# Kernel optimization log

Hardware: AMD Instinct MI355X
Metric: run time of the kernel (lower is better)

## Reference

```python
import jax, jax.numpy as jnp
import numpy as np
import math

NUM_HEADS = 16
WINDOW = 128  # telephone/sliding-window size: attend to self + previous WINDOW-1 tokens
EPS = 1e-6


def setup_inputs() -> dict:
    key = jax.random.key(0)
    k1, k2, k3, k4 = jax.random.split(key, 4)
    B, S, D = 4, 4096, 1024
    x = jax.random.normal(k1, (B, S, D), dtype=jnp.float32)
    g = jnp.ones((D,), dtype=jnp.float32)  # RMSNorm weight
    Wqkv = jax.random.normal(k2, (D, 3 * D), dtype=jnp.float32) * 0.02
    Wo = jax.random.normal(k3, (D, D), dtype=jnp.float32) * 0.02
    return {"x": x, "g": g, "Wqkv": Wqkv, "Wo": Wo}


def _telephone_block(x, g, Wqkv, Wo):
    B, S, D = x.shape
    H, dh, W = NUM_HEADS, D // NUM_HEADS, WINDOW
    nb = S // W  # number of key/query blocks

    # pre-RMSNorm
    xn = x * jax.lax.rsqrt(jnp.mean(x * x, axis=-1, keepdims=True) + EPS) * g

    # fused QKV projection
    qkv = xn @ Wqkv  # [B,S,3D]
    q, k, v = jnp.split(qkv, 3, axis=-1)

    def split_heads(t):
        # [B,S,D] -> [B,H,nb,W,dh]
        return t.reshape(B, nb, W, H, dh).transpose(0, 3, 1, 2, 4)

    q, k, v = split_heads(q), split_heads(k), split_heads(v)

    def shift_prev(t):
        # previous block of keys/values (zeros for block 0, masked below)
        return jnp.pad(t[:, :, :-1], ((0, 0), (0, 0), (1, 0), (0, 0), (0, 0)))

    k_ext = jnp.concatenate([shift_prev(k), k], axis=3)  # [B,H,nb,2W,dh]
    v_ext = jnp.concatenate([shift_prev(v), v], axis=3)

    scale = 1.0 / math.sqrt(dh)
    scores = jnp.einsum('bhnqd,bhnkd->bhnqk', q, k_ext) * scale  # [B,H,nb,W,2W]

    # sliding-window causal mask within the [prev-block, cur-block] key span.
    # query local pos i in [0,W); key extended pos j in [0,2W) maps to offset j-W.
    i = jnp.arange(W)[:, None]
    j = jnp.arange(2 * W)[None, :]
    base = (j > i) & (j <= i + W)          # last W tokens incl. self
    first = base & (j >= W)                # block 0 has no previous block
    blk0 = (jnp.arange(nb) == 0)[:, None, None]
    mask = jnp.where(blk0, first[None], base[None])  # [nb,W,2W]

    scores = jnp.where(mask[None, None], scores, jnp.finfo(scores.dtype).min)
    p = jax.nn.softmax(scores, axis=-1)
    o = jnp.einsum('bhnqk,bhnkd->bhnqd', p, v_ext)   # [B,H,nb,W,dh]
    o = o.transpose(0, 2, 3, 1, 4).reshape(B, S, D)
    h = o @ Wo
    return x + h  # residual


def reference(x, g, Wqkv, Wo):
    return _telephone_block(x, g, Wqkv, Wo)
```

## Files before the change

kernel.cpp:

```cpp
#include <hip/hip_runtime.h>
#include <hip/hip_bf16.h>


typedef __attribute__((ext_vector_type(8))) short s8v;
typedef __attribute__((ext_vector_type(4))) float f4v;

#define MFMA_BF16(A, B, C) __builtin_amdgcn_mfma_f32_16x16x32_bf16((A), (B), (C), 0, 0, 0)

static __device__ __forceinline__ void gload_lds16(const void* g, void* l) {
    __builtin_amdgcn_global_load_lds((const __attribute__((address_space(1))) void*)g,
                                     (__attribute__((address_space(3))) void*)l, 16, 0, 0);
}

static __device__ __forceinline__ unsigned short f2bf(float f) {
    return __builtin_bit_cast(unsigned short, __float2bfloat16(f));
}

__global__ __launch_bounds__(256) void transpose_cast_kernel(const float* __restrict__ in,
                                                             unsigned short* __restrict__ out,
                                                             int K, int N) {
    __shared__ float tile[32][33];
    int nbk = K >> 5;
    int bk = blockIdx.x % nbk;
    int bn = blockIdx.x / nbk;
    int tx = threadIdx.x & 31, ty = threadIdx.x >> 5;
#pragma unroll
    for (int i = 0; i < 4; i++) {
        int r = ty + i * 8;
        tile[r][tx] = in[(size_t)(bk * 32 + r) * N + bn * 32 + tx];
    }
    __syncthreads();
#pragma unroll
    for (int i = 0; i < 4; i++) {
        int r = ty + i * 8;
        out[(size_t)(bn * 32 + r) * K + bk * 32 + tx] = f2bf(tile[tx][r]);
    }
}

__global__ __launch_bounds__(256) void rmsnorm_kernel(const float* __restrict__ x,
                                                      const float* __restrict__ g,
                                                      unsigned short* __restrict__ xn) {
    const int D = 1024;
    int row = blockIdx.x;
    int t = threadIdx.x;
    float4 v = ((const float4*)(x + (size_t)row * D))[t];
    float ss = v.x * v.x + v.y * v.y + v.z * v.z + v.w * v.w;
#pragma unroll
    for (int off = 32; off >= 1; off >>= 1) ss += __shfl_xor(ss, off, 64);
    __shared__ float partials[4];
    if ((t & 63) == 0) partials[t >> 6] = ss;
    __syncthreads();
    float tot = partials[0] + partials[1] + partials[2] + partials[3];
    float scale = rsqrtf(tot * (1.0f / D) + 1e-6f);
    float4 gv = ((const float4*)g)[t];
    ushort4 o;
    o.x = f2bf(v.x * scale * gv.x);
    o.y = f2bf(v.y * scale * gv.y);
    o.z = f2bf(v.z * scale * gv.z);
    o.w = f2bf(v.w * scale * gv.w);
    ((ushort4*)xn)[(size_t)row * (D / 4) + t] = o;
}

template <int MODE>
__global__ __launch_bounds__(512, 2) void gemm256_kernel(const unsigned short* __restrict__ A,
                                                         const unsigned short* __restrict__ Bt,
                                                         unsigned short* __restrict__ Cb,
                                                         float* __restrict__ Cf,
                                                         const float* __restrict__ resid,
                                                         int M, int N, int K) {
    __shared__ __align__(16) char lds_s[98304];

    const int nbn = N >> 8;
    const int nwg = (M >> 8) * nbn;
    int bid = blockIdx.x;
    int cpx = nwg >> 3;
    int wg = (bid & 7) * cpx + (bid >> 3);
    int bm = wg / nbn, bn = wg % nbn;

    int tid = threadIdx.x, lane = tid & 63, w = tid >> 6;
    int wm = w >> 2, wn = w & 3;
    int hl = lane >> 4, ll = lane & 15;

    const unsigned short* Ab = A + (size_t)bm * 256 * K;
    const unsigned short* Bb = Bt + (size_t)bn * 256 * K;

    int lrow = lane >> 2;
    int sslot = ((lane & 3) ^ ((lane >> 3) & 3)) * 8;
    const unsigned short* gAw = Ab + (size_t)(w * 32 + lrow) * K + sslot;
    const unsigned short* gBw = Bb + (size_t)(w * 32 + lrow) * K + sslot;
    char* ldst = lds_s + w * 2048;

    int rslot = (hl ^ ((ll >> 1) & 3)) * 16;
    const char* ldsA = lds_s + (wm * 128 + ll) * 64 + rslot;
    const char* ldsB = lds_s + 16384 + (wn * 64 + ll) * 64 + rslot;

    const int NT = K >> 5;

    f4v acc[8][4] = {};

#define STAGE(t_) do {                                                                    \
        char* l_ = ldst + ((t_) % 3) * 32768;                                             \
        gload_lds16(gAw + (t_) * 32, l_);                                                 \
        gload_lds16(gAw + (t_) * 32 + 16 * K, l_ + 1024);                                 \
        gload_lds16(gBw + (t_) * 32, l_ + 16384);                                         \
        gload_lds16(gBw + (t_) * 32 + 16 * K, l_ + 16384 + 1024);                         \
    } while (0)

    STAGE(0);
    STAGE(1);
    asm volatile("s_waitcnt vmcnt(4)" ::: "memory");
    asm volatile("s_barrier" ::: "memory");

    for (int t = 0; t < NT; t++) {
        int bufo = (t % 3) * 32768;
        if (t + 2 < NT) STAGE(t + 2);
        const char* bufA = ldsA + bufo;
        const char* bufB = ldsB + bufo;
        s8v bf[4];
#pragma unroll
        for (int n = 0; n < 4; n++) bf[n] = *(const s8v*)(bufB + n * 1024);
        __builtin_amdgcn_s_setprio(1);
#pragma unroll
        for (int m = 0; m < 8; m++) {
            s8v am = *(const s8v*)(bufA + m * 1024);
#pragma unroll
            for (int n = 0; n < 4; n++) acc[m][n] = MFMA_BF16(am, bf[n], acc[m][n]);
        }
        __builtin_amdgcn_s_setprio(0);
        if (t + 1 < NT) {
            if (t + 2 < NT)
                asm volatile("s_waitcnt vmcnt(4) lgkmcnt(0)" ::: "memory");
            else
                asm volatile("s_waitcnt vmcnt(0) lgkmcnt(0)" ::: "memory");
            asm volatile("s_barrier" ::: "memory");
        }
    }
#undef STAGE

    int crow0 = bm * 256 + wm * 128;
    int ccol0 = bn * 256 + wn * 64;
#pragma unroll
    for (int m = 0; m < 8; m++) {
#pragma unroll
        for (int r = 0; r < 4; r++) {
            int row = crow0 + m * 16 + hl * 4 + r;
#pragma unroll
            for (int n = 0; n < 4; n++) {
                int col = ccol0 + n * 16 + ll;
                float val = acc[m][n][r];
                if (MODE == 0) {
                    Cb[(size_t)row * N + col] = f2bf(val);
                } else {
                    size_t idx = (size_t)row * N + col;
                    Cf[idx] = resid[idx] + val;
                }
            }
        }
    }
}

__global__ __launch_bounds__(256, 3) void attn_kernel(const unsigned short* __restrict__ qkv,
                                                      unsigned short* __restrict__ obuf) {
    constexpr int S = 4096, D = 1024, H = 16, W = 128, NB = 32;
    constexpr int TD = 3 * D;
    constexpr int PS = 40;

    __shared__ __align__(16) char smem[44032];
    unsigned short* KV = (unsigned short*)smem;

    int bid = blockIdx.x;
    int blk = bid % NB;
    int h = (bid / NB) % H;
    int b = bid / (NB * H);

    int tid = threadIdx.x, lane = tid & 63, w = tid >> 6;
    int hl = lane >> 4, ll = lane & 15;
    unsigned short* Ps = (unsigned short*)(smem + 33792) + w * 32 * PS;

    int kbase = blk * W - W;
    size_t rowbase = (size_t)(b * S);

    {
        int lr = lane >> 3;
        int scb = ((lane & 7) ^ lr) * 16;
#pragma unroll
        for (int r = 0; r < 8; r++) {
            int row = r * 32 + w * 8 + lr;
            int s = kbase + row;
            s = s < 0 ? 0 : s;
            const char* src = (const char*)(qkv + (rowbase + s) * TD + D + h * 64) + scb;
            char* dst = smem + (size_t)(r * 32 + w * 8) * 128 + lane * 16;
            gload_lds16(src, dst);
        }
    }

    s8v qf[2][2];
    {
        const unsigned short* qb = qkv + (rowbase + blk * W + w * 32) * TD + h * 64;
#pragma unroll
        for (int mf = 0; mf < 2; mf++)
#pragma unroll
            for (int ks = 0; ks < 2; ks++)
                qf[mf][ks] = *(const s8v*)(qb + (size_t)(mf * 16 + ll) * TD + ks * 32 + hl * 8);
    }

    s8v vreg[8];
    {
        int k0 = w * 64 + (lane >> 3) * 8;
        int d0 = (lane & 7) * 8;
#pragma unroll
        for (int it = 0; it < 8; it++) {
            int s = kbase + k0 + it;
            s = s < 0 ? 0 : s;
            vreg[it] = *(const s8v*)(qkv + (rowbase + s) * TD + 2 * D + h * 64 + d0);
        }
    }
    __syncthreads();

    f4v sc[2][9] = {};
    int g0 = w * 2;
    __builtin_amdgcn_s_setprio(1);
#pragma unroll
    for (int gi = 0; gi < 10; gi++) {
#pragma unroll
        for (int ks = 0; ks < 2; ks++) {
            int row = (g0 + gi) * 16 + ll;
            s8v kf = *(const s8v*)(smem + (size_t)row * 128 +
                                   (((unsigned)(ks * 64 + hl * 16)) ^ ((ll & 7) << 4)));
            if (gi < 9) sc[0][gi] = MFMA_BF16(qf[0][ks], kf, sc[0][gi]);
            if (gi > 0) sc[1][gi - 1] = MFMA_BF16(qf[1][ks], kf, sc[1][gi - 1]);
        }
    }
    __builtin_amdgcn_s_setprio(0);

    float linv[2][4];
#pragma unroll
    for (int mf = 0; mf < 2; mf++) {
#pragma unroll
        for (int r = 0; r < 4; r++) {
            int ip = hl * 4 + r;
            float mx = -1e30f;
#pragma unroll
            for (int nf = 0; nf < 9; nf++) {
                bool ok = (nf > 0 || ll > ip) && (nf < 8 || ll <= ip) &&
                          (blk > 0 || (g0 + mf + nf) >= 8);
                float sval = ok ? sc[mf][nf][r] * 0.125f : -1e30f;
                sc[mf][nf][r] = sval;
                mx = fmaxf(mx, sval);
            }
#pragma unroll
            for (int off = 1; off < 16; off <<= 1) mx = fmaxf(mx, __shfl_xor(mx, off, 64));
            float sum = 0.f;
#pragma unroll
            for (int nf = 0; nf < 9; nf++) {
                float p = __expf(sc[mf][nf][r] - mx);
                sc[mf][nf][r] = p;
                sum += p;
            }
#pragma unroll
            for (int off = 1; off < 16; off <<= 1) sum += __shfl_xor(sum, off, 64);
            linv[mf][r] = 1.f / sum;
        }
    }

    __syncthreads();

    {
        int k0 = w * 64 + (lane >> 3) * 8;
        int d0 = (lane & 7) * 8;
#pragma unroll
        for (int e = 0; e < 8; e++) {
            int d = d0 + e;
            s8v tmp;
#pragma unroll
            for (int i = 0; i < 8; i++) tmp[i] = vreg[i][e];
            *(s8v*)(KV + d * 264 + (k0 ^ (((d >> 3) & 7) << 3))) = tmp;
        }
    }
    __syncthreads();

    f4v o[2][4] = {};
#pragma unroll
    for (int c = 0; c < 5; c++) {
#pragma unroll
        for (int mf = 0; mf < 2; mf++) {
#pragma unroll
            for (int j16 = 0; j16 < 2; j16++) {
                int nf = c * 2 + j16 - mf;
                int nfc = nf < 0 ? 0 : (nf > 8 ? 8 : nf);
#pragma unroll
                for (int r = 0; r < 4; r++) {
                    float val = (nf >= 0 && nf < 9) ? sc[mf][nfc][r] : 0.f;
                    Ps[(mf * 16 + hl * 4 + r) * PS + j16 * 16 + ll] = f2bf(val);
                }
            }
        }
        asm volatile("s_waitcnt lgkmcnt(0)" ::: "memory");
        s8v pa[2];
        pa[0] = *(const s8v*)(Ps + ll * PS + hl * 8);
        pa[1] = *(const s8v*)(Ps + (16 + ll) * PS + hl * 8);
        int cb = (w + c) * 32;
        __builtin_amdgcn_s_setprio(1);
#pragma unroll
        for (int nd = 0; nd < 4; nd++) {
            int d = nd * 16 + ll;
            int kk = (cb + hl * 8) ^ (((d >> 3) & 7) << 3);
            s8v vb = *(const s8v*)(KV + d * 264 + kk);
            o[0][nd] = MFMA_BF16(pa[0], vb, o[0][nd]);
            o[1][nd] = MFMA_BF16(pa[1], vb, o[1][nd]);
        }
        __builtin_amdgcn_s_setprio(0);
    }

    unsigned short* ob = obuf + (rowbase + blk * W + w * 32) * D + h * 64;
#pragma unroll
    for (int mf = 0; mf < 2; mf++)
#pragma unroll
        for (int r = 0; r < 4; r++) {
            int row = mf * 16 + hl * 4 + r;
#pragma unroll
            for (int nd = 0; nd < 4; nd++)
                ob[(size_t)row * D + nd * 16 + ll] = f2bf(o[mf][nd][r] * linv[mf][r]);
        }
}

extern "C" void kernel_launch(void* const* d_in, const int* in_sizes, int n_in,
                              void* d_out, int out_size, void* d_ws, size_t ws_size,
                              hipStream_t stream) {
    const float* x = (const float*)d_in[0];
    const float* g = (const float*)d_in[1];
    const float* Wqkv = (const float*)d_in[2];
    const float* Wo = (const float*)d_in[3];
    float* out = (float*)d_out;

    const int S = 4096, D = 1024, B = 4;
    const int M = B * S;
    const int N3 = 3 * D;

    char* ws = (char*)d_ws;
    unsigned short* WqkvT = (unsigned short*)ws;
    unsigned short* WoT = (unsigned short*)(ws + 6291456);
    unsigned short* xn = (unsigned short*)(ws + 8388608);
    unsigned short* qkv = (unsigned short*)(ws + 41943040);

    transpose_cast_kernel<<<dim3((D / 32) * (N3 / 32)), dim3(256), 0, stream>>>(Wqkv, WqkvT, D, N3);
    transpose_cast_kernel<<<dim3((D / 32) * (D / 32)), dim3(256), 0, stream>>>(Wo, WoT, D, D);
    rmsnorm_kernel<<<dim3(M), dim3(256), 0, stream>>>(x, g, xn);
    gemm256_kernel<0><<<dim3((M / 256) * (N3 / 256)), dim3(512), 0, stream>>>(
        xn, WqkvT, qkv, nullptr, nullptr, M, N3, D);
    attn_kernel<<<dim3(B * 16 * (S / 128)), dim3(256), 0, stream>>>(qkv, xn);
    gemm256_kernel<1><<<dim3((M / 256) * (D / 256)), dim3(512), 0, stream>>>(
        xn, WoT, nullptr, out, x, M, D, D);
}
```

Measured before the change: 223.3 us.

## Deepen GEMM LDS pipeline to four stages and prefetch fragments into registers

The bf16 GEMM main loop moves from a three-buffer to a four-buffer LDS ring, so global loads are issued three tiles ahead. A and B fragments for the next tile are read from LDS into a second set of registers, interleaved with the current tile's MFMAs, and the loop is unrolled by two to swap register sets. The aim is to hide LDS read latency and global load latency behind matrix math. The cost is more LDS (128KB), more registers per thread, and a loop that assumes an even number of K tiles.

```diff
diff --git a/kernel.cpp b/kernel.cpp
--- a/kernel.cpp
+++ b/kernel.cpp
@@ -68,7 +68,7 @@
                                                          float* __restrict__ Cf,
                                                          const float* __restrict__ resid,
                                                          int M, int N, int K) {
-    __shared__ __align__(16) char lds_s[98304];
+    __shared__ __align__(16) char lds_s[131072];
 
     const int nbn = N >> 8;
     const int nwg = (M >> 8) * nbn;
@@ -88,53 +88,66 @@
     int sslot = ((lane & 3) ^ ((lane >> 3) & 3)) * 8;
     const unsigned short* gAw = Ab + (size_t)(w * 32 + lrow) * K + sslot;
     const unsigned short* gBw = Bb + (size_t)(w * 32 + lrow) * K + sslot;
-    char* ldst = lds_s + w * 2048;
 
     int rslot = (hl ^ ((ll >> 1) & 3)) * 16;
-    const char* ldsA = lds_s + (wm * 128 + ll) * 64 + rslot;
-    const char* ldsB = lds_s + 16384 + (wn * 64 + ll) * 64 + rslot;
+    const int ldsAoff = (wm * 128 + ll) * 64 + rslot;
+    const int ldsBoff = 16384 + (wn * 64 + ll) * 64 + rslot;
 
     const int NT = K >> 5;
 
     f4v acc[8][4] = {};
+    s8v aX[8], aY[8], bfr[4];
 
 #define STAGE(t_) do {                                                                    \
-        char* l_ = ldst + ((t_) % 3) * 32768;                                             \
-        gload_lds16(gAw + (t_) * 32, l_);                                                 \
-        gload_lds16(gAw + (t_) * 32 + 16 * K, l_ + 1024);                                 \
-        gload_lds16(gBw + (t_) * 32, l_ + 16384);                                         \
-        gload_lds16(gBw + (t_) * 32 + 16 * K, l_ + 16384 + 1024);                         \
+        char* l_ = lds_s + ((t_) & 3) * 32768 + w * 2048;                                 \
+        gload_lds16(gAw + (size_t)(t_) * 32, l_);                                         \
+        gload_lds16(gAw + (size_t)(t_) * 32 + 16 * K, l_ + 1024);                         \
+        gload_lds16(gBw + (size_t)(t_) * 32, l_ + 16384);                                 \
+        gload_lds16(gBw + (size_t)(t_) * 32 + 16 * K, l_ + 16384 + 1024);                 \
+    } while (0)
+
+#define TILE(CUR, NXT, t_) do {                                                           \
+        const char* nb_ = lds_s + (((t_) + 1) & 3) * 32768;                               \
+        if ((t_) + 1 < NT) {                                                              \
+            _Pragma("unroll") for (int m = 0; m < 8; m++)                                 \
+                NXT[m] = *(const s8v*)(nb_ + ldsAoff + m * 1024);                         \
+        }                                                                                 \
+        if ((t_) + 3 < NT) STAGE((t_) + 3);                                               \
+        __builtin_amdgcn_s_setprio(1);                                                    \
+        _Pragma("unroll") for (int n = 0; n < 4; n++) {                                   \
+            _Pragma("unroll") for (int m = 0; m < 8; m++)                                 \
+                acc[m][n] = MFMA_BF16(CUR[m], bfr[n], acc[m][n]);                         \
+            if ((t_) + 1 < NT)                                                            \
+                bfr[n] = *(const s8v*)(nb_ + ldsBoff + n * 1024);                         \
+        }                                                                                 \
+        __builtin_amdgcn_s_setprio(0);                                                    \
+        if ((t_) + 1 < NT) {                                                              \
+            if ((t_) + 3 < NT) asm volatile("s_waitcnt vmcnt(4)" ::: "memory");           \
+            else asm volatile("s_waitcnt vmcnt(0)" ::: "memory");                         \
+            asm volatile("s_barrier" ::: "memory");                                       \
+            __builtin_amdgcn_sched_barrier(0);                                            \
+        }                                                                                 \
     } while (0)
 
     STAGE(0);
     STAGE(1);
+    STAGE(2);
     asm volatile("s_waitcnt vmcnt(4)" ::: "memory");
     asm volatile("s_barrier" ::: "memory");
-
-    for (int t = 0; t < NT; t++) {
-        int bufo = (t % 3) * 32768;
-        if (t + 2 < NT) STAGE(t + 2);
-        const char* bufA = ldsA + bufo;
-        const char* bufB = ldsB + bufo;
-        s8v bf[4];
-#pragma unroll
-        for (int n = 0; n < 4; n++) bf[n] = *(const s8v*)(bufB + n * 1024);
-        __builtin_amdgcn_s_setprio(1);
-#pragma unroll
-        for (int m = 0; m < 8; m++) {
-            s8v am = *(const s8v*)(bufA + m * 1024);
-#pragma unroll
-            for (int n = 0; n < 4; n++) acc[m][n] = MFMA_BF16(am, bf[n], acc[m][n]);
-        }
-        __builtin_amdgcn_s_setprio(0);
-        if (t + 1 < NT) {
-            if (t + 2 < NT)
-                asm volatile("s_waitcnt vmcnt(4) lgkmcnt(0)" ::: "memory");
-            else
-                asm volatile("s_waitcnt vmcnt(0) lgkmcnt(0)" ::: "memory");
-            asm volatile("s_barrier" ::: "memory");
-        }
-    }
+    __builtin_amdgcn_sched_barrier(0);
+    {
+        const char* b0 = lds_s;
+#pragma unroll
+        for (int m = 0; m < 8; m++) aX[m] = *(const s8v*)(b0 + ldsAoff + m * 1024);
+#pragma unroll
+        for (int n = 0; n < 4; n++) bfr[n] = *(const s8v*)(b0 + ldsBoff + n * 1024);
+    }
+
+    for (int t = 0; t + 1 < NT; t += 2) {
+        TILE(aX, aY, t);
+        TILE(aY, aX, t + 1);
+    }
+#undef TILE
 #undef STAGE
 
     int crow0 = bm * 256 + wm * 128;
```

After: 217.7 us. 2.5% less time.

## Stream GEMM B operand directly from global memory and merge weight transpose launches

Applied to the files above, without the earlier changes.

The GEMM kernel now stages only the A tile in LDS, with double buffering over a K-step of 64, and loads B fragments straight from global memory into registers. Waves are rearranged into 4x2 with 64x128 output tiles per wave. The two weight transpose-cast launches are merged into one launch. This cuts LDS traffic and launch overhead, but B loads are no longer staged ahead, so global latency is exposed inside the loop, and the full vmcnt(0) wait each iteration reduces overlap.

```diff
diff --git a/kernel.cpp b/kernel.cpp
--- a/kernel.cpp
+++ b/kernel.cpp
@@ -16,13 +16,24 @@
     return __builtin_bit_cast(unsigned short, __float2bfloat16(f));
 }
 
-__global__ __launch_bounds__(256) void transpose_cast_kernel(const float* __restrict__ in,
-                                                             unsigned short* __restrict__ out,
-                                                             int K, int N) {
+__global__ __launch_bounds__(256) void transpose_cast_kernel(const float* __restrict__ Wqkv,
+                                                             unsigned short* __restrict__ WqkvT,
+                                                             const float* __restrict__ Wo,
+                                                             unsigned short* __restrict__ WoT) {
+    const int K = 1024;
+    int nb1 = (K >> 5) * (3072 >> 5);
+    const float* in;
+    unsigned short* out;
+    int N, bidx;
+    if (blockIdx.x < (unsigned)nb1) {
+        in = Wqkv; out = WqkvT; N = 3072; bidx = blockIdx.x;
+    } else {
+        in = Wo; out = WoT; N = 1024; bidx = blockIdx.x - nb1;
+    }
     __shared__ float tile[32][33];
     int nbk = K >> 5;
-    int bk = blockIdx.x % nbk;
-    int bn = blockIdx.x / nbk;
+    int bk = bidx % nbk;
+    int bn = bidx / nbk;
     int tx = threadIdx.x & 31, ty = threadIdx.x >> 5;
 #pragma unroll
     for (int i = 0; i < 4; i++) {
@@ -68,7 +79,7 @@
                                                          float* __restrict__ Cf,
                                                          const float* __restrict__ resid,
                                                          int M, int N, int K) {
-    __shared__ __align__(16) char lds_s[98304];
+    __shared__ __align__(16) char lds_s[65536];
 
     const int nbn = N >> 8;
     const int nwg = (M >> 8) * nbn;
@@ -78,76 +89,83 @@
     int bm = wg / nbn, bn = wg % nbn;
 
     int tid = threadIdx.x, lane = tid & 63, w = tid >> 6;
-    int wm = w >> 2, wn = w & 3;
+    int wm = w >> 1, wn = w & 1;
     int hl = lane >> 4, ll = lane & 15;
 
     const unsigned short* Ab = A + (size_t)bm * 256 * K;
     const unsigned short* Bb = Bt + (size_t)bn * 256 * K;
 
-    int lrow = lane >> 2;
-    int sslot = ((lane & 3) ^ ((lane >> 3) & 3)) * 8;
-    const unsigned short* gAw = Ab + (size_t)(w * 32 + lrow) * K + sslot;
-    const unsigned short* gBw = Bb + (size_t)(w * 32 + lrow) * K + sslot;
-    char* ldst = lds_s + w * 2048;
-
-    int rslot = (hl ^ ((ll >> 1) & 3)) * 16;
-    const char* ldsA = lds_s + (wm * 128 + ll) * 64 + rslot;
-    const char* ldsB = lds_s + 16384 + (wn * 64 + ll) * 64 + rslot;
-
-    const int NT = K >> 5;
-
-    f4v acc[8][4] = {};
-
-#define STAGE(t_) do {                                                                    \
-        char* l_ = ldst + ((t_) % 3) * 32768;                                             \
-        gload_lds16(gAw + (t_) * 32, l_);                                                 \
-        gload_lds16(gAw + (t_) * 32 + 16 * K, l_ + 1024);                                 \
-        gload_lds16(gBw + (t_) * 32, l_ + 16384);                                         \
-        gload_lds16(gBw + (t_) * 32 + 16 * K, l_ + 16384 + 1024);                         \
+    int srow = lane >> 3;
+    int scol = ((lane & 7) ^ srow) * 8;
+    const unsigned short* gA = Ab + (size_t)srow * K + scol;
+
+    int c0 = (hl * 16) ^ ((ll & 7) * 16);
+    const char* ldsA = lds_s + (wm * 64 + ll) * 128;
+
+    const unsigned short* gB = Bb + (size_t)(wn * 128 + ll) * K + hl * 8;
+
+    const int NT = K >> 6;
+
+    f4v acc[4][8] = {};
+
+#define STAGE_A(t_) do {                                                                  \
+        char* l_ = lds_s + ((t_) & 1) * 32768 + w * 1024;                                 \
+        const unsigned short* g_ = gA + (t_) * 64;                                        \
+        gload_lds16(g_ + (size_t)(w * 8) * K, l_);                                        \
+        gload_lds16(g_ + (size_t)(64 + w * 8) * K, l_ + 8192);                            \
+        gload_lds16(g_ + (size_t)(128 + w * 8) * K, l_ + 16384);                          \
+        gload_lds16(g_ + (size_t)(192 + w * 8) * K, l_ + 24576);                          \
     } while (0)
 
-    STAGE(0);
-    STAGE(1);
-    asm volatile("s_waitcnt vmcnt(4)" ::: "memory");
+    STAGE_A(0);
+    asm volatile("s_waitcnt vmcnt(0)" ::: "memory");
     asm volatile("s_barrier" ::: "memory");
 
     for (int t = 0; t < NT; t++) {
-        int bufo = (t % 3) * 32768;
-        if (t + 2 < NT) STAGE(t + 2);
-        const char* bufA = ldsA + bufo;
-        const char* bufB = ldsB + bufo;
-        s8v bf[4];
-#pragma unroll
-        for (int n = 0; n < 4; n++) bf[n] = *(const s8v*)(bufB + n * 1024);
+        if (t + 1 < NT) STAGE_A(t + 1);
+        const char* bufA = ldsA + (t & 1) * 32768;
+        s8v af[4][2];
+#pragma unroll
+        for (int m = 0; m < 4; m++) {
+            af[m][0] = *(const s8v*)(bufA + m * 2048 + c0);
+            af[m][1] = *(const s8v*)(bufA + m * 2048 + (c0 ^ 64));
+        }
+        s8v bf0[8], bf1[8];
+        const unsigned short* gBt = gB + t * 64;
+#pragma unroll
+        for (int nf = 0; nf < 8; nf++) bf0[nf] = *(const s8v*)(gBt + (size_t)nf * 16 * K);
+#pragma unroll
+        for (int nf = 0; nf < 8; nf++) bf1[nf] = *(const s8v*)(gBt + (size_t)nf * 16 * K + 32);
         __builtin_amdgcn_s_setprio(1);
 #pragma unroll
-        for (int m = 0; m < 8; m++) {
-            s8v am = *(const s8v*)(bufA + m * 1024);
-#pragma unroll
-            for (int n = 0; n < 4; n++) acc[m][n] = MFMA_BF16(am, bf[n], acc[m][n]);
-        }
+        for (int m = 0; m < 4; m++)
+#pragma unroll
+            for (int nf = 0; nf < 8; nf++)
+                acc[m][nf] = MFMA_BF16(af[m][0], bf0[nf], acc[m][nf]);
+#pragma unroll
+        for (int m = 0; m < 4; m++)
+#pragma unroll
+            for (int nf = 0; nf < 8; nf++)
+                acc[m][nf] = MFMA_BF16(af[m][1], bf1[nf], acc[m][nf]);
         __builtin_amdgcn_s_setprio(0);
         if (t + 1 < NT) {
-            if (t + 2 < NT)
-                asm volatile("s_waitcnt vmcnt(4) lgkmcnt(0)" ::: "memory");
-            else
-                asm volatile("s_waitcnt vmcnt(0) lgkmcnt(0)" ::: "memory");
+            asm volatile("s_waitcnt vmcnt(0) lgkmcnt(0)" ::: "memory");
             asm volatile("s_barrier" ::: "memory");
         }
     }
-#undef STAGE
-
-    int crow0 = bm * 256 + wm * 128;
-    int ccol0 = bn * 256 + wn * 64;
-#pragma unroll
-    for (int m = 0; m < 8; m++) {
+#undef STAGE_A
+
+    int crow0 = bm * 256 + wm * 64;
+    int ccol0 = bn * 256 + wn * 128;
+#pragma unroll
+    for (int m = 0; m < 4; m++) {
 #pragma unroll
         for (int r = 0; r < 4; r++) {
             int row = crow0 + m * 16 + hl * 4 + r;
 #pragma unroll
-            for (int n = 0; n < 4; n++) {
-                int col = ccol0 + n * 16 + ll;
-                float val = acc[m][n][r];
+            for (int nf = 0; nf < 8; nf++) {
+                int col = ccol0 + nf * 16 + ll;
+                float val = acc[m][nf][r];
                 if (MODE == 0) {
                     Cb[(size_t)row * N + col] = f2bf(val);
                 } else {
@@ -343,8 +361,8 @@
     unsigned short* xn = (unsigned short*)(ws + 8388608);
     unsigned short* qkv = (unsigned short*)(ws + 41943040);
 
-    transpose_cast_kernel<<<dim3((D / 32) * (N3 / 32)), dim3(256), 0, stream>>>(Wqkv, WqkvT, D, N3);
-    transpose_cast_kernel<<<dim3((D / 32) * (D / 32)), dim3(256), 0, stream>>>(Wo, WoT, D, D);
+    transpose_cast_kernel<<<dim3((D / 32) * (N3 / 32) + (D / 32) * (D / 32)), dim3(256), 0,
+                            stream>>>(Wqkv, WqkvT, Wo, WoT);
     rmsnorm_kernel<<<dim3(M), dim3(256), 0, stream>>>(x, g, xn);
     gemm256_kernel<0><<<dim3((M / 256) * (N3 / 256)), dim3(512), 0, stream>>>(
         xn, WqkvT, qkv, nullptr, nullptr, M, N3, D);
```

Result: slower. 391.2 us (+75.2%).
